# Performance work log

Measured on AMD Instinct MI355X. Metric: run time of the kernel, lower is better.

Reference implementation:

```python
import jax, jax.numpy as jnp
import numpy as np

HEADS = 4


def _dwconv(x, w, d):
    # x: (B,C,H,W), w: (C,1,3,3); reflection pad by d then dilated depthwise conv (same spatial size)
    xp = jnp.pad(x, ((0, 0), (0, 0), (d, d), (d, d)), mode='reflect')
    return jax.lax.conv_general_dilated(
        xp, w, window_strides=(1, 1), padding='VALID', rhs_dilation=(d, d),
        feature_group_count=x.shape[1], dimension_numbers=('NCHW', 'OIHW', 'NCHW'))


def _pyramid(x, w1, w2, w3):
    x0, x1, x2, x3 = jnp.split(x, 4, axis=1)
    return jnp.concatenate(
        [x0, _dwconv(x1, w1, 1), _dwconv(x2, w2, 2), _dwconv(x3, w3, 3)], axis=1)


def _conv1x1(x, w):
    return jnp.einsum('oi,bihw->bohw', w, x)


def _heads(t):
    # b (H c) h w -> b H c (h w)
    b, C, h, w = t.shape
    return t.reshape(b, HEADS, C // HEADS, h * w)


def _l2norm(t):
    # torch F.normalize(dim=-1): x / max(||x||, eps)
    return t / jnp.maximum(jnp.linalg.norm(t, axis=-1, keepdims=True), 1e-12)


def setup_inputs() -> dict:
    key = jax.random.key(0)
    ks = jax.random.split(key, 20)
    B, H, W = 2, 256, 256
    dim, dim_h, dim_l, sque = 256, 128, 64, 4
    s = 0.05
    inp = {
        'x':   jax.random.normal(ks[0], (B, dim, H, W), jnp.float32),
        'x_h': jax.random.normal(ks[1], (B, dim_h, H, W), jnp.float32),
        'x_l': jax.random.normal(ks[2], (B, dim_l, H, W), jnp.float32),
        # kv: 1x1 conv dim -> dim//sque*2 = 128, pyramid dw on 128 ch (32 per branch)
        'w_kv':  jax.random.normal(ks[3], (dim // sque * 2, dim), jnp.float32) * s,
        'kv_dw1': jax.random.normal(ks[4], (32, 1, 3, 3), jnp.float32) * s,
        'kv_dw2': jax.random.normal(ks[5], (32, 1, 3, 3), jnp.float32) * s,
        'kv_dw3': jax.random.normal(ks[6], (32, 1, 3, 3), jnp.float32) * s,
        # q_h: dim_h -> 32, pyramid branches of 8 ch
        'w_qh':  jax.random.normal(ks[7], (dim_h // sque, dim_h), jnp.float32) * s,
        'qh_dw1': jax.random.normal(ks[8], (8, 1, 3, 3), jnp.float32) * s,
        'qh_dw2': jax.random.normal(ks[9], (8, 1, 3, 3), jnp.float32) * s,
        'qh_dw3': jax.random.normal(ks[10], (8, 1, 3, 3), jnp.float32) * s,
        # q_l: dim_l -> 16, pyramid branches of 4 ch
        'w_ql':  jax.random.normal(ks[11], (dim_l // sque, dim_l), jnp.float32) * s,
        'ql_dw1': jax.random.normal(ks[12], (4, 1, 3, 3), jnp.float32) * s,
        'ql_dw2': jax.random.normal(ks[13], (4, 1, 3, 3), jnp.float32) * s,
        'ql_dw3': jax.random.normal(ks[14], (4, 1, 3, 3), jnp.float32) * s,
        'w_ph': jax.random.normal(ks[15], (dim_h, dim_h // sque), jnp.float32) * s,
        'w_pl': jax.random.normal(ks[16], (dim_l, dim_l // sque), jnp.float32) * s,
        'temperature': jnp.ones((HEADS, 1, 1), jnp.float32),
    }
    return inp


def reference(x, x_h, x_l, w_kv, kv_dw1, kv_dw2, kv_dw3,
              w_qh, qh_dw1, qh_dw2, qh_dw3,
              w_ql, ql_dw1, ql_dw2, ql_dw3,
              w_ph, w_pl, temperature):
    b, _, h, w = x.shape
    kv = _pyramid(_conv1x1(x, w_kv), kv_dw1, kv_dw2, kv_dw3)
    k, v = jnp.split(kv, 2, axis=1)
    q_h = _pyramid(_conv1x1(x_h, w_qh), qh_dw1, qh_dw2, qh_dw3)
    q_l = _pyramid(_conv1x1(x_l, w_ql), ql_dw1, ql_dw2, ql_dw3)
    k = _l2norm(_heads(k))      # (b, H, ck, N)
    v = _heads(v)               # (b, H, ck, N)
    q_h = _l2norm(_heads(q_h))  # (b, H, ch, N)
    q_l = _l2norm(_heads(q_l))  # (b, H, cl, N)
    temp = temperature[None]    # (1, H, 1, 1)

    def attend(q):
        a = jnp.einsum('bhcn,bhdn->bhcd', q, k) * temp  # channel-wise scores
        a = jax.nn.softmax(a, axis=-1)
        return jnp.einsum('bhcd,bhdn->bhcn', a, v)

    msg_h = attend(q_h).reshape(b, -1, h, w)
    msg_l = attend(q_l).reshape(b, -1, h, w)
    return _conv1x1(msg_h, w_ph), _conv1x1(msg_l, w_pl)
```

## Files before the change

kernel.cpp:

```cpp
#include <hip/hip_runtime.h>
#include <hip/hip_bf16.h>


#define NPIX 65536

using bf16x8 = __attribute__((ext_vector_type(8))) short;
using f32x4  = __attribute__((ext_vector_type(4))) float;

__device__ __forceinline__ unsigned short f2bf(float f) {
    unsigned u = __builtin_bit_cast(unsigned, f);
    u = u + 0x7FFF + ((u >> 16) & 1);
    return (unsigned short)(u >> 16);
}

__global__ void zero_k(float* __restrict__ p, int n) {
    int i = blockIdx.x * 256 + threadIdx.x;
    if (i < n) p[i] = 0.f;
}

__global__ void cast_w_k(const float* __restrict__ w_kv,
                         const float* __restrict__ w_qh,
                         const float* __restrict__ w_ql,
                         unsigned short* __restrict__ wkv_b,
                         unsigned short* __restrict__ wqh_b,
                         unsigned short* __restrict__ wql_b) {
    int idx = blockIdx.x * 256 + threadIdx.x;
    if (idx < 32768) wkv_b[idx] = f2bf(w_kv[idx]);
    else if (idx < 32768 + 4096) wqh_b[idx - 32768] = f2bf(w_qh[idx - 32768]);
    else if (idx < 32768 + 4096 + 1024) wql_b[idx - 36864] = f2bf(w_ql[idx - 36864]);
}

template <int MW, int MSPLIT, int KT, int CPB, bool SPLIT>
__global__ __launch_bounds__(256) void gemm_mfma_k(
    const float* __restrict__ src, const unsigned short* __restrict__ A,
    float* __restrict__ out, float* __restrict__ out2,
    long srcBStride, long aBStride, long outBStride, long out2BStride) {
    constexpr int K  = KT * 32;
    constexpr int RW = K / 2 + 4;
    constexpr int NW = MSPLIT;

    __shared__ unsigned Blds[64 * RW];

    const int t    = threadIdx.x;
    const int wave = t >> 6;
    const int lane = t & 63;
    const int r    = lane & 15;
    const int q    = lane >> 4;

    const int chunk0 = blockIdx.x * CPB;
    const int b      = chunk0 >> 10;
    const int m0     = (wave % MSPLIT) * MW * 16;
    const int nb     = (wave / MSPLIT) * NW * 16;

    bf16x8 af[MW][KT];
    {
        const unsigned short* Ab = A + (size_t)b * aBStride;
#pragma unroll
        for (int mw = 0; mw < MW; ++mw)
#pragma unroll
            for (int kt = 0; kt < KT; ++kt)
                af[mw][kt] = *(const bf16x8*)(Ab + (size_t)(m0 + mw * 16 + r) * K + kt * 32 + q * 8);
    }

    const float* srcb = src + (size_t)b * srcBStride;

    for (int cc = 0; cc < CPB; ++cc) {
        const int chunk = chunk0 + cc;
        const int n0 = (chunk & 1023) * 64;

        {
            const int sn = t & 63, kp0 = t >> 6;
            const float* sp = srcb + n0 + sn;
#pragma unroll
            for (int it = 0; it < K / 8; ++it) {
                const int kp = it * 4 + kp0;
                const float v0 = sp[(size_t)(2 * kp) * NPIX];
                const float v1 = sp[(size_t)(2 * kp + 1) * NPIX];
                Blds[sn * RW + kp] = (unsigned)f2bf(v0) | ((unsigned)f2bf(v1) << 16);
            }
        }
        __syncthreads();

        f32x4 acc[MW][NW];
#pragma unroll
        for (int mw = 0; mw < MW; ++mw)
#pragma unroll
            for (int nw = 0; nw < NW; ++nw) acc[mw][nw] = (f32x4){0.f, 0.f, 0.f, 0.f};

#pragma unroll
        for (int kt = 0; kt < KT; ++kt) {
            bf16x8 bf[NW];
#pragma unroll
            for (int nw = 0; nw < NW; ++nw) {
                const int n = nb + nw * 16 + r;
                bf[nw] = *(const bf16x8*)(&Blds[n * RW + kt * 16 + q * 4]);
            }
#pragma unroll
            for (int mw = 0; mw < MW; ++mw)
#pragma unroll
                for (int nw = 0; nw < NW; ++nw)
                    acc[mw][nw] = __builtin_amdgcn_mfma_f32_16x16x32_bf16(
                        af[mw][kt], bf[nw], acc[mw][nw], 0, 0, 0);
        }

#pragma unroll
        for (int mw = 0; mw < MW; ++mw) {
            const int obase = m0 + mw * 16 + q * 4;
#pragma unroll
            for (int nw = 0; nw < NW; ++nw) {
                const int n = n0 + nb + nw * 16 + r;
#pragma unroll
                for (int rr = 0; rr < 4; ++rr) {
                    const int o = obase + rr;
                    float* dst;
                    if (SPLIT && o >= 128)
                        dst = out2 + (size_t)b * out2BStride + (size_t)(o - 128) * NPIX + n;
                    else
                        dst = out + (size_t)b * outBStride + (size_t)o * NPIX + n;
                    *dst = acc[mw][nw][rr];
                }
            }
        }
        __syncthreads();
    }
}

__device__ __forceinline__ int refl(int p) {
    return (p < 0) ? -p : ((p > 255) ? 510 - p : p);
}

__global__ __launch_bounds__(256) void pyramid_k(const float* __restrict__ in,
                                                 float* __restrict__ out, int C,
                                                 const float* __restrict__ w1,
                                                 const float* __restrict__ w2,
                                                 const float* __restrict__ w3) {
    const int t = threadIdx.x;
    const int bi = blockIdx.x;
    const int y = bi & 255;
    const int bc = bi >> 8;
    const int G = C >> 2;
    const int c = bc % C;
    const int g = (c >= 3 * G) ? 3 : (c >= 2 * G) ? 2 : (c >= G) ? 1 : 0;

    const float* src = in + (size_t)bc * NPIX;
    const size_t oidx = (size_t)bi * 256 + t;

    if (g == 0) {
        out[oidx] = src[y * 256 + t];
        return;
    }
    const float* wp = (g == 1 ? w1 : (g == 2 ? w2 : w3)) + (c - g * G) * 9;
    float s = 0.f;
#pragma unroll
    for (int ky = 0; ky < 3; ++ky) {
        const int yy = refl(y + (ky - 1) * g);
        const float* rowp = src + yy * 256;
#pragma unroll
        for (int kx = 0; kx < 3; ++kx) {
            const int xx = refl(t + (kx - 1) * g);
            s = fmaf(wp[ky * 3 + kx], rowp[xx], s);
        }
    }
    out[oidx] = s;
}

__global__ __launch_bounds__(256) void scores_k(const float* __restrict__ qh,
                                                const float* __restrict__ ql,
                                                const float* __restrict__ kv,
                                                float* __restrict__ Sbuf) {
    __shared__ float qs[12 * 513];
    __shared__ float ks[16 * 513];
    const int t = threadIdx.x;
    const int slice = blockIdx.x;
    const int hd = blockIdx.y;
    const int b = blockIdx.z;
    const int n0 = slice * 2048;

    const float* pa = nullptr;
    const float* pb = nullptr;
    if (t < 192) {
        int c = t >> 4, d = t & 15;
        pa = qs + c * 513;
        pb = ks + d * 513;
    } else if (t < 208) {
        int d = t - 192;
        pa = ks + d * 513;
        pb = pa;
    } else if (t < 220) {
        int c = t - 208;
        pa = qs + c * 513;
        pb = pa;
    }

    float acc = 0.f;
    for (int cb = 0; cb < 4; ++cb) {
        const int base = n0 + cb * 512;
        for (int idx = t; idx < 28 * 512; idx += 256) {
            const int row = idx >> 9, i = idx & 511;
            const float* src;
            if (row < 8)
                src = qh + (size_t)(b * 32 + hd * 8 + row) * NPIX;
            else if (row < 12)
                src = ql + (size_t)(b * 16 + hd * 4 + (row - 8)) * NPIX;
            else
                src = kv + (size_t)(b * 128 + hd * 16 + (row - 12)) * NPIX;
            const float v = src[base + i];
            if (row < 12)
                qs[row * 513 + i] = v;
            else
                ks[(row - 12) * 513 + i] = v;
        }
        __syncthreads();
        if (pa) {
#pragma unroll 8
            for (int i = 0; i < 512; ++i) acc = fmaf(pa[i], pb[i], acc);
        }
        __syncthreads();
    }

    if (t < 192) {
        int c = t >> 4, d = t & 15;
        atomicAdd(&Sbuf[((b * 4 + hd) * 12 + c) * 16 + d], acc);
    } else if (t < 208) {
        int d = t - 192;
        atomicAdd(&Sbuf[1536 + (b * 4 + hd) * 16 + d], acc);
    } else if (t < 220) {
        int c = t - 208;
        atomicAdd(&Sbuf[1664 + (b * 4 + hd) * 12 + c], acc);
    }
}

__global__ __launch_bounds__(256) void finalize_k(const float* __restrict__ Sbuf,
                                                  const float* __restrict__ w_ph,
                                                  const float* __restrict__ w_pl,
                                                  const float* __restrict__ temp,
                                                  unsigned short* __restrict__ CT) {
    __shared__ float As[192];
    const int t = threadIdx.x;
    const int hd = blockIdx.x;
    const int b = blockIdx.y;

    if (t < 192) {
        const int c = t >> 4, d = t & 15;
        const float kss = Sbuf[1536 + (b * 4 + hd) * 16 + d];
        const float qss = Sbuf[1664 + (b * 4 + hd) * 12 + c];
        const float invk = 1.f / fmaxf(sqrtf(kss), 1e-12f);
        const float invq = 1.f / fmaxf(sqrtf(qss), 1e-12f);
        float s = Sbuf[((b * 4 + hd) * 12 + c) * 16 + d] * invq * invk * temp[hd];
        float m = s;
        for (int mask = 8; mask >= 1; mask >>= 1) m = fmaxf(m, __shfl_xor(m, mask, 16));
        const float e = expf(s - m);
        float sum = e;
        for (int mask = 8; mask >= 1; mask >>= 1) sum += __shfl_xor(sum, mask, 16);
        As[c * 16 + d] = e / sum;
    }
    __syncthreads();

    unsigned short* CTb = CT + (size_t)b * 192 * 64;
    for (int idx = t; idx < 3072; idx += 256) {
        const int d = idx & 15, rr = idx >> 4;
        float s = 0.f;
        if (rr < 128) {
#pragma unroll
            for (int c = 0; c < 8; ++c)
                s = fmaf(w_ph[rr * 32 + hd * 8 + c], As[c * 16 + d], s);
        } else {
            const int r2 = rr - 128;
#pragma unroll
            for (int c = 0; c < 4; ++c)
                s = fmaf(w_pl[r2 * 16 + hd * 4 + c], As[(8 + c) * 16 + d], s);
        }
        CTb[(size_t)rr * 64 + hd * 16 + d] = f2bf(s);
    }
}

extern "C" void kernel_launch(void* const* d_in, const int* in_sizes, int n_in,
                              void* d_out, int out_size, void* d_ws, size_t ws_size,
                              hipStream_t stream) {
    const float* x      = (const float*)d_in[0];
    const float* x_h    = (const float*)d_in[1];
    const float* x_l    = (const float*)d_in[2];
    const float* w_kv   = (const float*)d_in[3];
    const float* kv_dw1 = (const float*)d_in[4];
    const float* kv_dw2 = (const float*)d_in[5];
    const float* kv_dw3 = (const float*)d_in[6];
    const float* w_qh   = (const float*)d_in[7];
    const float* qh_dw1 = (const float*)d_in[8];
    const float* qh_dw2 = (const float*)d_in[9];
    const float* qh_dw3 = (const float*)d_in[10];
    const float* w_ql   = (const float*)d_in[11];
    const float* ql_dw1 = (const float*)d_in[12];
    const float* ql_dw2 = (const float*)d_in[13];
    const float* ql_dw3 = (const float*)d_in[14];
    const float* w_ph   = (const float*)d_in[15];
    const float* w_pl   = (const float*)d_in[16];
    const float* temp   = (const float*)d_in[17];
    float* out = (float*)d_out;

    char* ws = (char*)d_ws;
    float*          Sbuf  = (float*)(ws + 0);
    unsigned short* wkv_b = (unsigned short*)(ws + 8192);
    unsigned short* wqh_b = (unsigned short*)(ws + 73728);
    unsigned short* wql_b = (unsigned short*)(ws + 81920);
    unsigned short* CT    = (unsigned short*)(ws + 90112);
    float* kvraw = (float*)(ws + 262144);
    float* kvpyr = (float*)(ws + 262144 + 67108864);
    float* qhraw = (float*)(ws + 262144 + 2 * 67108864);
    float* qhpyr = (float*)(ws + 262144 + 2 * 67108864 + 16777216);
    float* qlraw = (float*)(ws + 262144 + 2 * 67108864 + 2 * 16777216);
    float* qlpyr = (float*)(ws + 262144 + 2 * 67108864 + 2 * 16777216 + 8388608);

    zero_k<<<7, 256, 0, stream>>>(Sbuf, 1760);
    cast_w_k<<<148, 256, 0, stream>>>(w_kv, w_qh, w_ql, wkv_b, wqh_b, wql_b);

    gemm_mfma_k<4, 2, 8, 4, false><<<512, 256, 0, stream>>>(
        x, wkv_b, kvraw, nullptr, 256L * NPIX, 0L, 128L * NPIX, 0L);
    gemm_mfma_k<2, 1, 4, 4, false><<<512, 256, 0, stream>>>(
        x_h, wqh_b, qhraw, nullptr, 128L * NPIX, 0L, 32L * NPIX, 0L);
    gemm_mfma_k<1, 1, 2, 4, false><<<512, 256, 0, stream>>>(
        x_l, wql_b, qlraw, nullptr, 64L * NPIX, 0L, 16L * NPIX, 0L);

    pyramid_k<<<65536, 256, 0, stream>>>(kvraw, kvpyr, 128, kv_dw1, kv_dw2, kv_dw3);
    pyramid_k<<<16384, 256, 0, stream>>>(qhraw, qhpyr, 32, qh_dw1, qh_dw2, qh_dw3);
    pyramid_k<<<8192, 256, 0, stream>>>(qlraw, qlpyr, 16, ql_dw1, ql_dw2, ql_dw3);

    scores_k<<<dim3(32, 4, 2), 256, 0, stream>>>(qhpyr, qlpyr, kvpyr, Sbuf);
    finalize_k<<<dim3(4, 2), 256, 0, stream>>>(Sbuf, w_ph, w_pl, temp, CT);

    gemm_mfma_k<6, 2, 2, 4, true><<<512, 256, 0, stream>>>(
        kvpyr + 64L * NPIX, CT, out, out + 2L * 128 * NPIX,
        128L * NPIX, 192L * 64, 128L * NPIX, 64L * NPIX);
}
```

Before: 479.7 us.

## Store pyramid outputs in bf16, use MFMA for scores, restructure GEMM grid

Pyramid outputs are now written as bf16 instead of fp32, which halves the traffic for the scores pass and the final projection GEMM. The projection GEMM reads those bf16 values directly. The pyramid kernel stages its three source rows in shared memory. The scores kernel drops the scalar LDS dot products and uses MFMA on bf16 inputs, computing the squared norms in the same pass. The GEMMs launch one 64-pixel chunk per block across 2048 blocks with a changed wave split. The cost is extra bf16 rounding on the intermediates and on the normalization sums.

Result: faster. 452.3 us (-5.7%).

```diff
diff --git a/kernel.cpp b/kernel.cpp
--- a/kernel.cpp
+++ b/kernel.cpp
@@ -1,5 +1,4 @@
 #include <hip/hip_runtime.h>
-#include <hip/hip_bf16.h>
 
 
 #define NPIX 65536
@@ -11,6 +10,9 @@
     unsigned u = __builtin_bit_cast(unsigned, f);
     u = u + 0x7FFF + ((u >> 16) & 1);
     return (unsigned short)(u >> 16);
+}
+__device__ __forceinline__ float bf2f(unsigned short u) {
+    return __builtin_bit_cast(float, (unsigned)u << 16);
 }
 
 __global__ void zero_k(float* __restrict__ p, int n) {
@@ -30,9 +32,9 @@
     else if (idx < 32768 + 4096 + 1024) wql_b[idx - 36864] = f2bf(w_ql[idx - 36864]);
 }
 
-template <int MW, int MSPLIT, int KT, int CPB, bool SPLIT>
+template <int MW, int MSPLIT, int KT, bool SPLIT, bool SRCBF>
 __global__ __launch_bounds__(256) void gemm_mfma_k(
-    const float* __restrict__ src, const unsigned short* __restrict__ A,
+    const void* __restrict__ srcv, const unsigned short* __restrict__ A,
     float* __restrict__ out, float* __restrict__ out2,
     long srcBStride, long aBStride, long outBStride, long out2BStride) {
     constexpr int K  = KT * 32;
@@ -47,10 +49,11 @@
     const int r    = lane & 15;
     const int q    = lane >> 4;
 
-    const int chunk0 = blockIdx.x * CPB;
-    const int b      = chunk0 >> 10;
-    const int m0     = (wave % MSPLIT) * MW * 16;
-    const int nb     = (wave / MSPLIT) * NW * 16;
+    const int chunk = blockIdx.x;
+    const int b     = chunk >> 10;
+    const int n0    = (chunk & 1023) * 64;
+    const int m0    = (wave % MSPLIT) * MW * 16;
+    const int nb    = (wave / MSPLIT) * NW * 16;
 
     bf16x8 af[MW][KT];
     {
@@ -62,15 +65,19 @@
                 af[mw][kt] = *(const bf16x8*)(Ab + (size_t)(m0 + mw * 16 + r) * K + kt * 32 + q * 8);
     }
 
-    const float* srcb = src + (size_t)b * srcBStride;
-
-    for (int cc = 0; cc < CPB; ++cc) {
-        const int chunk = chunk0 + cc;
-        const int n0 = (chunk & 1023) * 64;
-
-        {
-            const int sn = t & 63, kp0 = t >> 6;
-            const float* sp = srcb + n0 + sn;
+    {
+        const int sn = t >> 2, kp0 = t & 3;
+        if constexpr (SRCBF) {
+            const unsigned short* sp = (const unsigned short*)srcv + (size_t)b * srcBStride + n0 + sn;
+#pragma unroll
+            for (int it = 0; it < K / 8; ++it) {
+                const int kp = it * 4 + kp0;
+                const unsigned v0 = sp[(size_t)(2 * kp) * NPIX];
+                const unsigned v1 = sp[(size_t)(2 * kp + 1) * NPIX];
+                Blds[sn * RW + kp] = v0 | (v1 << 16);
+            }
+        } else {
+            const float* sp = (const float*)srcv + (size_t)b * srcBStride + n0 + sn;
 #pragma unroll
             for (int it = 0; it < K / 8; ++it) {
                 const int kp = it * 4 + kp0;
@@ -79,49 +86,48 @@
                 Blds[sn * RW + kp] = (unsigned)f2bf(v0) | ((unsigned)f2bf(v1) << 16);
             }
         }
-        __syncthreads();
-
-        f32x4 acc[MW][NW];
+    }
+    __syncthreads();
+
+    f32x4 acc[MW][NW];
+#pragma unroll
+    for (int mw = 0; mw < MW; ++mw)
+#pragma unroll
+        for (int nw = 0; nw < NW; ++nw) acc[mw][nw] = (f32x4){0.f, 0.f, 0.f, 0.f};
+
+#pragma unroll
+    for (int kt = 0; kt < KT; ++kt) {
+        bf16x8 bf[NW];
+#pragma unroll
+        for (int nw = 0; nw < NW; ++nw) {
+            const int n = nb + nw * 16 + r;
+            bf[nw] = *(const bf16x8*)(&Blds[n * RW + kt * 16 + q * 4]);
+        }
 #pragma unroll
         for (int mw = 0; mw < MW; ++mw)
 #pragma unroll
-            for (int nw = 0; nw < NW; ++nw) acc[mw][nw] = (f32x4){0.f, 0.f, 0.f, 0.f};
-
-#pragma unroll
-        for (int kt = 0; kt < KT; ++kt) {
-            bf16x8 bf[NW];
-#pragma unroll
-            for (int nw = 0; nw < NW; ++nw) {
-                const int n = nb + nw * 16 + r;
-                bf[nw] = *(const bf16x8*)(&Blds[n * RW + kt * 16 + q * 4]);
+            for (int nw = 0; nw < NW; ++nw)
+                acc[mw][nw] = __builtin_amdgcn_mfma_f32_16x16x32_bf16(
+                    af[mw][kt], bf[nw], acc[mw][nw], 0, 0, 0);
+    }
+
+#pragma unroll
+    for (int mw = 0; mw < MW; ++mw) {
+        const int obase = m0 + mw * 16 + q * 4;
+#pragma unroll
+        for (int nw = 0; nw < NW; ++nw) {
+            const int n = n0 + nb + nw * 16 + r;
+#pragma unroll
+            for (int rr = 0; rr < 4; ++rr) {
+                const int o = obase + rr;
+                float* dst;
+                if (SPLIT && o >= 128)
+                    dst = out2 + (size_t)b * out2BStride + (size_t)(o - 128) * NPIX + n;
+                else
+                    dst = out + (size_t)b * outBStride + (size_t)o * NPIX + n;
+                *dst = acc[mw][nw][rr];
             }
-#pragma unroll
-            for (int mw = 0; mw < MW; ++mw)
-#pragma unroll
-                for (int nw = 0; nw < NW; ++nw)
-                    acc[mw][nw] = __builtin_amdgcn_mfma_f32_16x16x32_bf16(
-                        af[mw][kt], bf[nw], acc[mw][nw], 0, 0, 0);
-        }
-
-#pragma unroll
-        for (int mw = 0; mw < MW; ++mw) {
-            const int obase = m0 + mw * 16 + q * 4;
-#pragma unroll
-            for (int nw = 0; nw < NW; ++nw) {
-                const int n = n0 + nb + nw * 16 + r;
-#pragma unroll
-                for (int rr = 0; rr < 4; ++rr) {
-                    const int o = obase + rr;
-                    float* dst;
-                    if (SPLIT && o >= 128)
-                        dst = out2 + (size_t)b * out2BStride + (size_t)(o - 128) * NPIX + n;
-                    else
-                        dst = out + (size_t)b * outBStride + (size_t)o * NPIX + n;
-                    *dst = acc[mw][nw][rr];
-                }
-            }
-        }
-        __syncthreads();
+        }
     }
 }
 
@@ -130,7 +136,7 @@
 }
 
 __global__ __launch_bounds__(256) void pyramid_k(const float* __restrict__ in,
-                                                 float* __restrict__ out, int C,
+                                                 unsigned short* __restrict__ out, int C,
                                                  const float* __restrict__ w1,
                                                  const float* __restrict__ w2,
                                                  const float* __restrict__ w3) {
@@ -143,90 +149,94 @@
     const int g = (c >= 3 * G) ? 3 : (c >= 2 * G) ? 2 : (c >= G) ? 1 : 0;
 
     const float* src = in + (size_t)bc * NPIX;
-    const size_t oidx = (size_t)bi * 256 + t;
+    const size_t oidx = (size_t)bc * NPIX + y * 256 + t;
 
     if (g == 0) {
-        out[oidx] = src[y * 256 + t];
+        out[oidx] = f2bf(src[y * 256 + t]);
         return;
     }
+
+    __shared__ float rows[3][256];
+    const int y0 = refl(y - g), y2 = refl(y + g);
+    for (int i = t; i < 384; i += 256) {
+        const int rr  = i >> 7;
+        const int off = (i & 127) * 2;
+        const int yy  = (rr == 0) ? y0 : (rr == 1) ? y : y2;
+        const float2 v = *(const float2*)(src + yy * 256 + off);
+        rows[rr][off] = v.x;
+        rows[rr][off + 1] = v.y;
+    }
+    __syncthreads();
+
     const float* wp = (g == 1 ? w1 : (g == 2 ? w2 : w3)) + (c - g * G) * 9;
+    const int xm = refl(t - g), xp = refl(t + g);
     float s = 0.f;
 #pragma unroll
     for (int ky = 0; ky < 3; ++ky) {
-        const int yy = refl(y + (ky - 1) * g);
-        const float* rowp = src + yy * 256;
-#pragma unroll
-        for (int kx = 0; kx < 3; ++kx) {
-            const int xx = refl(t + (kx - 1) * g);
-            s = fmaf(wp[ky * 3 + kx], rowp[xx], s);
-        }
-    }
-    out[oidx] = s;
-}
-
-__global__ __launch_bounds__(256) void scores_k(const float* __restrict__ qh,
-                                                const float* __restrict__ ql,
-                                                const float* __restrict__ kv,
+        s = fmaf(wp[ky * 3 + 0], rows[ky][xm], s);
+        s = fmaf(wp[ky * 3 + 1], rows[ky][t], s);
+        s = fmaf(wp[ky * 3 + 2], rows[ky][xp], s);
+    }
+    out[oidx] = f2bf(s);
+}
+
+__global__ __launch_bounds__(256) void scores_k(const unsigned short* __restrict__ qhp,
+                                                const unsigned short* __restrict__ qlp,
+                                                const unsigned short* __restrict__ kvp,
                                                 float* __restrict__ Sbuf) {
-    __shared__ float qs[12 * 513];
-    __shared__ float ks[16 * 513];
     const int t = threadIdx.x;
+    const int wave = t >> 6, lane = t & 63;
+    const int r = lane & 15, q = lane >> 4;
     const int slice = blockIdx.x;
     const int hd = blockIdx.y;
     const int b = blockIdx.z;
-    const int n0 = slice * 2048;
-
-    const float* pa = nullptr;
-    const float* pb = nullptr;
+
+    const unsigned short* qrow;
+    if (r < 8)       qrow = qhp + (size_t)(b * 32 + hd * 8 + r) * NPIX;
+    else if (r < 12) qrow = qlp + (size_t)(b * 16 + hd * 4 + (r - 8)) * NPIX;
+    else             qrow = qhp + (size_t)(b * 32 + hd * 8) * NPIX;
+    const unsigned short* krow = kvp + (size_t)(b * 128 + hd * 16 + r) * NPIX;
+
+    const int base = slice * 1024 + wave * 256;
+    f32x4 acc = (f32x4){0.f, 0.f, 0.f, 0.f};
+    float qq = 0.f, kk = 0.f;
+#pragma unroll
+    for (int c8 = 0; c8 < 8; ++c8) {
+        const int n = base + c8 * 32 + q * 8;
+        const bf16x8 a  = *(const bf16x8*)(qrow + n);
+        const bf16x8 bb = *(const bf16x8*)(krow + n);
+        acc = __builtin_amdgcn_mfma_f32_16x16x32_bf16(a, bb, acc, 0, 0, 0);
+#pragma unroll
+        for (int j = 0; j < 8; ++j) {
+            const float av = bf2f((unsigned short)a[j]);
+            const float bv = bf2f((unsigned short)bb[j]);
+            qq = fmaf(av, av, qq);
+            kk = fmaf(bv, bv, kk);
+        }
+    }
+    qq += __shfl_xor(qq, 16); qq += __shfl_xor(qq, 32);
+    kk += __shfl_xor(kk, 16); kk += __shfl_xor(kk, 32);
+
+    __shared__ float Sred[4][16][16];
+    __shared__ float qred[4][16];
+    __shared__ float kred[4][16];
+#pragma unroll
+    for (int rr = 0; rr < 4; ++rr) Sred[wave][q * 4 + rr][r] = acc[rr];
+    if (q == 0) { qred[wave][r] = qq; kred[wave][r] = kk; }
+    __syncthreads();
+
     if (t < 192) {
-        int c = t >> 4, d = t & 15;
-        pa = qs + c * 513;
-        pb = ks + d * 513;
+        const int c = t >> 4, d = t & 15;
+        const float s = Sred[0][c][d] + Sred[1][c][d] + Sred[2][c][d] + Sred[3][c][d];
+        if (c < 12) atomicAdd(&Sbuf[((b * 4 + hd) * 12 + c) * 16 + d], s);
     } else if (t < 208) {
-        int d = t - 192;
-        pa = ks + d * 513;
-        pb = pa;
+        const int d = t - 192;
+        const float s = kred[0][d] + kred[1][d] + kred[2][d] + kred[3][d];
+        atomicAdd(&Sbuf[1536 + (b * 4 + hd) * 16 + d], s);
     } else if (t < 220) {
-        int c = t - 208;
-        pa = qs + c * 513;
-        pb = pa;
-    }
-
-    float acc = 0.f;
-    for (int cb = 0; cb < 4; ++cb) {
-        const int base = n0 + cb * 512;
-        for (int idx = t; idx < 28 * 512; idx += 256) {
-            const int row = idx >> 9, i = idx & 511;
-            const float* src;
-            if (row < 8)
-                src = qh + (size_t)(b * 32 + hd * 8 + row) * NPIX;
-            else if (row < 12)
-                src = ql + (size_t)(b * 16 + hd * 4 + (row - 8)) * NPIX;
-            else
-                src = kv + (size_t)(b * 128 + hd * 16 + (row - 12)) * NPIX;
-            const float v = src[base + i];
-            if (row < 12)
-                qs[row * 513 + i] = v;
-            else
-                ks[(row - 12) * 513 + i] = v;
-        }
-        __syncthreads();
-        if (pa) {
-#pragma unroll 8
-            for (int i = 0; i < 512; ++i) acc = fmaf(pa[i], pb[i], acc);
-        }
-        __syncthreads();
-    }
-
-    if (t < 192) {
-        int c = t >> 4, d = t & 15;
-        atomicAdd(&Sbuf[((b * 4 + hd) * 12 + c) * 16 + d], acc);
-    } else if (t < 208) {
-        int d = t - 192;
-        atomicAdd(&Sbuf[1536 + (b * 4 + hd) * 16 + d], acc);
-    } else if (t < 220) {
-        int c = t - 208;
-        atomicAdd(&Sbuf[1664 + (b * 4 + hd) * 12 + c], acc);
+        const int c = t - 208;
+        const float s = qred[0][c] + qred[1][c] + qred[2][c] + qred[3][c];
+        atomicAdd(&Sbuf[1664 + (b * 4 + hd) * 12 + c], s);
     }
 }
 
@@ -303,31 +313,31 @@
     unsigned short* wqh_b = (unsigned short*)(ws + 73728);
     unsigned short* wql_b = (unsigned short*)(ws + 81920);
     unsigned short* CT    = (unsigned short*)(ws + 90112);
-    float* kvraw = (float*)(ws + 262144);
-    float* kvpyr = (float*)(ws + 262144 + 67108864);
-    float* qhraw = (float*)(ws + 262144 + 2 * 67108864);
-    float* qhpyr = (float*)(ws + 262144 + 2 * 67108864 + 16777216);
-    float* qlraw = (float*)(ws + 262144 + 2 * 67108864 + 2 * 16777216);
-    float* qlpyr = (float*)(ws + 262144 + 2 * 67108864 + 2 * 16777216 + 8388608);
+    float*          kvraw = (float*)(ws + 262144);
+    float*          qhraw = (float*)(ws + 67371008);
+    float*          qlraw = (float*)(ws + 84148224);
+    unsigned short* kvpyr = (unsigned short*)(ws + 92536832);
+    unsigned short* qhpyr = (unsigned short*)(ws + 126091264);
+    unsigned short* qlpyr = (unsigned short*)(ws + 134479872);
 
     zero_k<<<7, 256, 0, stream>>>(Sbuf, 1760);
     cast_w_k<<<148, 256, 0, stream>>>(w_kv, w_qh, w_ql, wkv_b, wqh_b, wql_b);
 
-    gemm_mfma_k<4, 2, 8, 4, false><<<512, 256, 0, stream>>>(
+    gemm_mfma_k<2, 4, 8, false, false><<<2048, 256, 0, stream>>>(
         x, wkv_b, kvraw, nullptr, 256L * NPIX, 0L, 128L * NPIX, 0L);
-    gemm_mfma_k<2, 1, 4, 4, false><<<512, 256, 0, stream>>>(
+    gemm_mfma_k<2, 1, 4, false, false><<<2048, 256, 0, stream>>>(
         x_h, wqh_b, qhraw, nullptr, 128L * NPIX, 0L, 32L * NPIX, 0L);
-    gemm_mfma_k<1, 1, 2, 4, false><<<512, 256, 0, stream>>>(
+    gemm_mfma_k<1, 1, 2, false, false><<<2048, 256, 0, stream>>>(
         x_l, wql_b, qlraw, nullptr, 64L * NPIX, 0L, 16L * NPIX, 0L);
 
     pyramid_k<<<65536, 256, 0, stream>>>(kvraw, kvpyr, 128, kv_dw1, kv_dw2, kv_dw3);
     pyramid_k<<<16384, 256, 0, stream>>>(qhraw, qhpyr, 32, qh_dw1, qh_dw2, qh_dw3);
     pyramid_k<<<8192, 256, 0, stream>>>(qlraw, qlpyr, 16, ql_dw1, ql_dw2, ql_dw3);
 
-    scores_k<<<dim3(32, 4, 2), 256, 0, stream>>>(qhpyr, qlpyr, kvpyr, Sbuf);
+    scores_k<<<dim3(64, 4, 2), 256, 0, stream>>>(qhpyr, qlpyr, kvpyr, Sbuf);
     finalize_k<<<dim3(4, 2), 256, 0, stream>>>(Sbuf, w_ph, w_pl, temp, CT);
 
-    gemm_mfma_k<6, 2, 2, 4, true><<<512, 256, 0, stream>>>(
-        kvpyr + 64L * NPIX, CT, out, out + 2L * 128 * NPIX,
+    gemm_mfma_k<3, 4, 2, true, true><<<2048, 256, 0, stream>>>(
+        (const void*)(kvpyr + 64L * NPIX), CT, out, out + 2L * 128 * NPIX,
         128L * NPIX, 192L * 64, 128L * NPIX, 64L * NPIX);
 }
```
